# Performance work log

Measured on AMD Instinct MI355X. Metric: run time of the kernel, lower is better.

## Reference

```python
import jax, jax.numpy as jnp
import numpy as np

B, T, D = 128, 512, 400
N_VALS, N_ACTS = 1024, 128

def setup_inputs() -> dict:
    key = jax.random.key(0)
    ks = jax.random.split(key, 7)
    H_utt = jax.random.normal(ks[0], (B, T, D), dtype=jnp.float32)
    c_utt = jax.random.normal(ks[1], (B, D), dtype=jnp.float32)
    C_acts = jax.random.normal(ks[2], (B, N_ACTS, D), dtype=jnp.float32)
    C_vals = jax.random.normal(ks[3], (N_VALS, 1, D), dtype=jnp.float32)
    W_score = jax.random.normal(ks[4], (1, D), dtype=jnp.float32) * (1.0 / np.sqrt(D))
    b_score = jnp.zeros((1,), dtype=jnp.float32)
    lens = jax.random.randint(ks[5], (B,), T // 2, T + 1, dtype=jnp.int64 if jax.config.read('jax_enable_x64') else jnp.int32)
    lens = lens.at[0].set(T)  # ensure max(lens) == T so masking matches torch semantics
    return {"H_utt": H_utt, "c_utt": c_utt, "C_acts": C_acts, "C_vals": C_vals,
            "W_score": W_score, "b_score": b_score, "utterance_len": lens}

def reference(H_utt, c_utt, C_acts, C_vals, W_score, b_score, utterance_len):
    vals = C_vals[:, 0, :]                                   # [V, D]
    # --- y_utts: default attention of each value vector over utterance states ---
    scores = jnp.einsum('btd,vd->bvt', H_utt, vals)          # mul+sum scoring
    mask = jnp.arange(T)[None, :] < utterance_len[:, None]   # [B, T]
    scores = jnp.where(mask[:, None, :], scores, -jnp.inf)
    probs = jax.nn.softmax(scores, axis=-1)                  # [B, V, T]
    q_utts = jnp.einsum('bvt,btd->bvd', probs, H_utt)        # weighted sum contexts
    y_utts = jnp.einsum('bvd,d->bv', q_utts, W_score[0]) + b_score[0]  # utt_scorer
    # --- y_acts: attention of c_utt over per-example act vectors, then score vs vals ---
    s2 = jnp.einsum('bad,bd->ba', C_acts, c_utt)
    p2 = jax.nn.softmax(s2, axis=-1)
    q_acts = jnp.einsum('ba,bad->bd', p2, C_acts)            # [B, D]
    y_acts = q_acts @ vals.T                                 # [B, V]
    return (y_utts, y_acts)
```

## Files before the change

### kernel.cpp

```cpp
#include <hip/hip_runtime.h>
#include <hip/hip_bf16.h>

#define B_  128
#define T_  512
#define D_  400
#define NV  1024
#define NA  128

#define TILE_BYTES 13312
#define MAIN_BLOCKS 512

#define LDH  424
#define NT   32
#define FB_MAIN_BLOCKS 1024

typedef __bf16 bf16_t;
typedef bf16_t bf16x8 __attribute__((ext_vector_type(8)));
typedef bf16_t bf16x4 __attribute__((ext_vector_type(4)));
typedef float  floatx4 __attribute__((ext_vector_type(4)));

__device__ inline float dot4(float4 a, float4 b) {
    return a.x * b.x + a.y * b.y + a.z * b.z + a.w * b.w;
}

__global__ __launch_bounds__(256) void prep_kernel(const float* __restrict__ H,
                                                   const float* __restrict__ W,
                                                   const float* __restrict__ Ca,
                                                   const float* __restrict__ cu,
                                                   float* __restrict__ hw,
                                                   bf16_t* __restrict__ Hf,
                                                   float* __restrict__ s2) {
    int wave = threadIdx.x >> 6;
    int lane = threadIdx.x & 63;
    if (blockIdx.x < 1024) {
        int tile = blockIdx.x * 4 + wave;
        int b = tile >> 5, ti = tile & 31;
        int lrow = lane & 15, quad = lane >> 4;
        const float* hrow = H + ((size_t)b * T_ + ti * 16 + lrow) * D_;
        char* fdst = (char*)Hf + (size_t)tile * TILE_BYTES + lane * 16;
        float acc = 0.f;
#pragma unroll
        for (int kk = 0; kk < 13; ++kk) {
            int k0 = kk * 32 + quad * 8;
            bf16x8 f;
            if (k0 < D_) {
                float4 x = *(const float4*)(hrow + k0);
                float4 y = *(const float4*)(hrow + k0 + 4);
                float4 wx = *(const float4*)(W + k0);
                float4 wy = *(const float4*)(W + k0 + 4);
                acc += dot4(x, wx) + dot4(y, wy);
                f[0] = (bf16_t)x.x; f[1] = (bf16_t)x.y; f[2] = (bf16_t)x.z; f[3] = (bf16_t)x.w;
                f[4] = (bf16_t)y.x; f[5] = (bf16_t)y.y; f[6] = (bf16_t)y.z; f[7] = (bf16_t)y.w;
            } else {
#pragma unroll
                for (int j = 0; j < 8; ++j) f[j] = (bf16_t)0.0f;
            }
            *(bf16x8*)(fdst + kk * 1024) = f;
        }
        acc += __shfl_xor(acc, 16, 64);
        acc += __shfl_xor(acc, 32, 64);
        if (lane < 16) hw[b * T_ + ti * 16 + lane] = acc;
    } else {
        long row = (long)(blockIdx.x - 1024) * 4 + wave;
        int b = (int)(row >> 7);
        const float4* a4 = (const float4*)(Ca + row * (long)D_);
        const float4* c4 = (const float4*)(cu + (long)b * D_);
        float acc = dot4(a4[lane], c4[lane]);
        if (lane < 36) acc += dot4(a4[lane + 64], c4[lane + 64]);
#pragma unroll
        for (int off = 1; off < 64; off <<= 1) acc += __shfl_xor(acc, off, 64);
        if (lane == 0) s2[row] = acc;
    }
}

__global__ __launch_bounds__(256) void qacts_kernel(const float* __restrict__ s2,
                                                    const float* __restrict__ Ca,
                                                    float* __restrict__ q_ws) {
    __shared__ float p_lds[NA];
    __shared__ float red[8];
    __shared__ __align__(16) float4 part[100];
    int b = blockIdx.x;
    int tid = threadIdx.x, wave = tid >> 6, lane = tid & 63;

    float s = (tid < NA) ? s2[(long)b * NA + tid] : -3.0e38f;
    float m = s;
#pragma unroll
    for (int off = 1; off < 64; off <<= 1) m = fmaxf(m, __shfl_xor(m, off, 64));
    if (lane == 0) red[wave] = m;
    __syncthreads();
    m = fmaxf(red[0], red[1]);
    float e = (tid < NA) ? __expf(s - m) : 0.f;
    float sum = e;
#pragma unroll
    for (int off = 1; off < 64; off <<= 1) sum += __shfl_xor(sum, off, 64);
    if (lane == 0) red[4 + wave] = sum;
    __syncthreads();
    float S = red[4] + red[5];
    if (tid < NA) p_lds[tid] = e / S;
    __syncthreads();

    int c4 = tid % 100;
    int half = tid / 100;
    float4 acc0 = {0.f, 0.f, 0.f, 0.f};
    if (tid < 200) {
        const float4* Cb4 = (const float4*)(Ca + (size_t)b * NA * D_);
        float4 acc1 = {0.f, 0.f, 0.f, 0.f};
        int a0 = half * 64;
#pragma unroll 4
        for (int a = 0; a < 64; a += 2) {
            float p0 = p_lds[a0 + a], p1 = p_lds[a0 + a + 1];
            float4 x0 = Cb4[(size_t)(a0 + a) * 100 + c4];
            float4 x1 = Cb4[(size_t)(a0 + a + 1) * 100 + c4];
            acc0.x += p0 * x0.x; acc0.y += p0 * x0.y; acc0.z += p0 * x0.z; acc0.w += p0 * x0.w;
            acc1.x += p1 * x1.x; acc1.y += p1 * x1.y; acc1.z += p1 * x1.z; acc1.w += p1 * x1.w;
        }
        acc0.x += acc1.x; acc0.y += acc1.y; acc0.z += acc1.z; acc0.w += acc1.w;
        if (half == 1) part[c4] = acc0;
    }
    __syncthreads();
    if (tid < 100) {
        float4 o = part[c4];
        o.x += acc0.x; o.y += acc0.y; o.z += acc0.z; o.w += acc0.w;
        ((float4*)(q_ws + (size_t)b * D_))[c4] = o;
    }
}

#define LDTILE(BUF, TI)                                                        \
    _Pragma("unroll") for (int kk = 0; kk < 13; ++kk)                          \
        BUF[kk] = *(const bf16x8*)(fb + (size_t)(TI) * TILE_BYTES + kk * 1024);

#define COMPUTE(BUF, TI)                                                       \
    do {                                                                       \
        floatx4 c_[4];                                                         \
        _Pragma("unroll") for (int s_ = 0; s_ < 4; ++s_) c_[s_] = zero4;       \
        _Pragma("unroll") for (int kk = 0; kk < 13; ++kk) {                    \
            bf16x8 bb_ = BUF[kk];                                              \
            _Pragma("unroll") for (int s_ = 0; s_ < 4; ++s_)                   \
                c_[s_] = __builtin_amdgcn_mfma_f32_16x16x32_bf16(              \
                    afrag[s_][kk], bb_, c_[s_], 0, 0, 0);                      \
        }                                                                      \
        int t_ = (TI) * 16 + lrow;                                             \
        float hwv_ = hwb[t_];                                                  \
        bool ok_ = t_ < len;                                                   \
        float cm_ = -3.0e38f;                                                  \
        _Pragma("unroll") for (int s_ = 0; s_ < 4; ++s_)                       \
            _Pragma("unroll") for (int r_ = 0; r_ < 4; ++r_) {                 \
                float v_ = ok_ ? c_[s_][r_] : -3.0e38f;                        \
                c_[s_][r_] = v_;                                               \
                cm_ = fmaxf(cm_, v_);                                          \
            }                                                                  \
        float mn_ = fmaxf(m_s, cm_);                                           \
        float alpha_ = __expf(m_s - mn_);                                      \
        m_s = mn_;                                                             \
        _Pragma("unroll") for (int s_ = 0; s_ < 4; ++s_)                       \
            _Pragma("unroll") for (int r_ = 0; r_ < 4; ++r_) {                 \
                float p_ = __expf(c_[s_][r_] - mn_);                           \
                l_s[s_][r_] = l_s[s_][r_] * alpha_ + p_;                       \
                a_s[s_][r_] = a_s[s_][r_] * alpha_ + p_ * hwv_;                \
            }                                                                  \
    } while (0)

__global__ __launch_bounds__(256, 1) void main_kernel(const bf16_t* __restrict__ Hf,
                                                      const float* __restrict__ Cv,
                                                      const float* __restrict__ hw,
                                                      const float* __restrict__ bs,
                                                      const int* __restrict__ lens,
                                                      const float* __restrict__ q_ws,
                                                      float* __restrict__ out) {
    int tid = threadIdx.x;
    int wave = tid >> 6, lane = tid & 63;

    if (blockIdx.x >= MAIN_BLOCKS) {
        long grp = (long)(blockIdx.x - MAIN_BLOCKS) * 4 + wave;
        int b = (int)(grp >> 8);
        int v0 = (int)(grp & 255) * 4;
        const float4* q4 = (const float4*)(q_ws + (size_t)b * D_);
        float4 qa = q4[lane];
        float4 qb = (lane < 36) ? q4[lane + 64] : make_float4(0.f, 0.f, 0.f, 0.f);
        float acc[4];
#pragma unroll
        for (int r = 0; r < 4; ++r) {
            const float4* v4 = (const float4*)(Cv + (size_t)(v0 + r) * D_);
            acc[r] = dot4(v4[lane], qa);
            if (lane < 36) acc[r] += dot4(v4[lane + 64], qb);
        }
#pragma unroll
        for (int off = 1; off < 64; off <<= 1) {
#pragma unroll
            for (int r = 0; r < 4; ++r) acc[r] += __shfl_xor(acc[r], off, 64);
        }
        if (lane == 0) {
            float4 o = make_float4(acc[0], acc[1], acc[2], acc[3]);
            *(float4*)(out + (size_t)B_ * NV + (size_t)b * NV + v0) = o;
        }
        return;
    }

    int i = blockIdx.x;
    int xcd = i & 7, vc = (i >> 3) & 3, bb = i >> 5;
    int b = xcd + 8 * bb;
    int vbase = vc * 256 + wave * 64;

    int lrow = lane & 15, quad = lane >> 4;
    int len = lens[b];
    float b0 = bs[0];

    bf16x8 afrag[4][13];
#pragma unroll
    for (int set = 0; set < 4; ++set) {
        const float* vrow = Cv + (size_t)(vbase + set * 16 + lrow) * D_;
#pragma unroll
        for (int kk = 0; kk < 13; ++kk) {
            int k0 = kk * 32 + quad * 8;
            bf16x8 f;
            if (k0 >= D_) {
#pragma unroll
                for (int j = 0; j < 8; ++j) f[j] = (bf16_t)0.0f;
            } else {
                const float4* p = (const float4*)(vrow + k0);
                float4 x = p[0], y = p[1];
                f[0] = (bf16_t)x.x; f[1] = (bf16_t)x.y;
                f[2] = (bf16_t)x.z; f[3] = (bf16_t)x.w;
                f[4] = (bf16_t)y.x; f[5] = (bf16_t)y.y;
                f[6] = (bf16_t)y.z; f[7] = (bf16_t)y.w;
            }
            afrag[set][kk] = f;
        }
    }

    float m_s = -3.0e38f;
    float l_s[4][4], a_s[4][4];
#pragma unroll
    for (int s = 0; s < 4; ++s)
#pragma unroll
        for (int r = 0; r < 4; ++r) { l_s[s][r] = 0.f; a_s[s][r] = 0.f; }

    const floatx4 zero4 = {0.f, 0.f, 0.f, 0.f};
    const float* hwb = hw + (size_t)b * T_;
    const char* fb = (const char*)Hf + (size_t)b * 32 * TILE_BYTES + lane * 16;

    int ntiles = (len + 15) >> 4;
    bf16x8 bfA[13], bfB[13];

    LDTILE(bfA, 0);
    int ti = 0;
    while (true) {
        if (ti + 1 < ntiles) { LDTILE(bfB, ti + 1); }
        COMPUTE(bfA, ti);
        ++ti; if (ti == ntiles) break;
        if (ti + 1 < ntiles) { LDTILE(bfA, ti + 1); }
        COMPUTE(bfB, ti);
        ++ti; if (ti == ntiles) break;
    }

#pragma unroll
    for (int s = 0; s < 4; ++s)
#pragma unroll
        for (int r = 0; r < 4; ++r) {
            float m = m_s, l = l_s[s][r], a = a_s[s][r];
#pragma unroll
            for (int off = 1; off < 16; off <<= 1) {
                float mo = __shfl_xor(m, off, 64);
                float lo = __shfl_xor(l, off, 64);
                float ao = __shfl_xor(a, off, 64);
                float mx = fmaxf(m, mo);
                float f1 = __expf(m - mx), f2 = __expf(mo - mx);
                l = l * f1 + lo * f2;
                a = a * f1 + ao * f2;
                m = mx;
            }
            if (lrow == 0) {
                int v = vbase + s * 16 + quad * 4 + r;
                out[(size_t)b * NV + v] = a / l + b0;
            }
        }
}

__global__ __launch_bounds__(256) void prep_fb_kernel(const float* __restrict__ H,
                                                      const float* __restrict__ W,
                                                      const float* __restrict__ Ca,
                                                      const float* __restrict__ cu,
                                                      float* __restrict__ hw,
                                                      float* __restrict__ s2) {
    int wave = threadIdx.x >> 6;
    int lane = threadIdx.x & 63;
    if (blockIdx.x < B_ * T_ / 4) {
        long row = (long)blockIdx.x * 4 + wave;
        const float* h = H + row * D_;
        float acc = 0.f;
        for (int k = lane; k < D_; k += 64) acc += h[k] * W[k];
#pragma unroll
        for (int off = 1; off < 64; off <<= 1) acc += __shfl_xor(acc, off, 64);
        if (lane == 0) hw[row] = acc;
    } else {
        long row = (long)(blockIdx.x - B_ * T_ / 4) * 4 + wave;
        int b = (int)(row >> 7);
        const float4* a4 = (const float4*)(Ca + row * (long)D_);
        const float4* c4 = (const float4*)(cu + (long)b * D_);
        float acc = dot4(a4[lane], c4[lane]);
        if (lane < 36) acc += dot4(a4[lane + 64], c4[lane + 64]);
#pragma unroll
        for (int off = 1; off < 64; off <<= 1) acc += __shfl_xor(acc, off, 64);
        if (lane == 0) s2[row] = acc;
    }
}

__global__ __launch_bounds__(256, 2) void main_fb_kernel(const float* __restrict__ H,
                                                         const float* __restrict__ Cv,
                                                         const float* __restrict__ hw,
                                                         const float* __restrict__ bs,
                                                         const int* __restrict__ lens,
                                                         const float* __restrict__ q_ws,
                                                         float* __restrict__ out) {
    __shared__ bf16_t h_lds[NT * LDH];
    __shared__ float hw_lds[NT];

    int tid = threadIdx.x;
    int wave = tid >> 6, lane = tid & 63;

    if (blockIdx.x >= FB_MAIN_BLOCKS) {
        long grp = (long)(blockIdx.x - FB_MAIN_BLOCKS) * 4 + wave;
        int b = (int)(grp >> 8);
        int v0 = (int)(grp & 255) * 4;
        const float4* q4 = (const float4*)(q_ws + (size_t)b * D_);
        float4 qa = q4[lane];
        float4 qb = (lane < 36) ? q4[lane + 64] : make_float4(0.f, 0.f, 0.f, 0.f);
        float acc[4];
#pragma unroll
        for (int r = 0; r < 4; ++r) {
            const float4* v4 = (const float4*)(Cv + (size_t)(v0 + r) * D_);
            acc[r] = dot4(v4[lane], qa);
            if (lane < 36) acc[r] += dot4(v4[lane + 64], qb);
        }
#pragma unroll
        for (int off = 1; off < 64; off <<= 1) {
#pragma unroll
            for (int r = 0; r < 4; ++r) acc[r] += __shfl_xor(acc[r], off, 64);
        }
        if (lane == 0) {
            float4 o = make_float4(acc[0], acc[1], acc[2], acc[3]);
            *(float4*)(out + (size_t)B_ * NV + (size_t)b * NV + v0) = o;
        }
        return;
    }

    int i = blockIdx.x;
    int xcd = i & 7, vc = (i >> 3) & 7, bb = i >> 6;
    int b = xcd + 8 * bb;
    int vbase = vc * 128;

    int lrow = lane & 15, quad = lane >> 4;
    int len = lens[b];
    float b0 = bs[0];

    for (int idx = tid; idx < NT * (LDH - D_); idx += 256) {
        int r = idx / (LDH - D_), c = idx % (LDH - D_);
        h_lds[r * LDH + D_ + c] = (bf16_t)0.0f;
    }

    bf16x8 afrag[2][13];
#pragma unroll
    for (int set = 0; set < 2; ++set) {
        const float* vrow = Cv + (size_t)(vbase + wave * 32 + set * 16 + lrow) * D_;
#pragma unroll
        for (int kk = 0; kk < 13; ++kk) {
            int k0 = kk * 32 + quad * 8;
            bf16x8 f;
            if (k0 >= D_) {
#pragma unroll
                for (int j = 0; j < 8; ++j) f[j] = (bf16_t)0.0f;
            } else {
                const float4* p = (const float4*)(vrow + k0);
                float4 x = p[0], y = p[1];
                f[0] = (bf16_t)x.x; f[1] = (bf16_t)x.y;
                f[2] = (bf16_t)x.z; f[3] = (bf16_t)x.w;
                f[4] = (bf16_t)y.x; f[5] = (bf16_t)y.y;
                f[6] = (bf16_t)y.z; f[7] = (bf16_t)y.w;
            }
            afrag[set][kk] = f;
        }
    }

    float m_s = -3.0e38f;
    float l_s[2][4], a_s[2][4];
#pragma unroll
    for (int set = 0; set < 2; ++set)
#pragma unroll
        for (int r = 0; r < 4; ++r) { l_s[set][r] = 0.f; a_s[set][r] = 0.f; }

    int ntiles = (len + NT - 1) / NT;
    const float* Hb = H + (size_t)b * T_ * D_;

    for (int tt = 0; tt < ntiles; ++tt) {
        int t0 = tt * NT;
        __syncthreads();
        for (int idx = tid; idx < NT * (D_ / 4); idx += 256) {
            int r = idx / (D_ / 4), c4 = idx % (D_ / 4);
            float4 x = *(const float4*)(Hb + (size_t)(t0 + r) * D_ + c4 * 4);
            bf16x4 f;
            f[0] = (bf16_t)x.x; f[1] = (bf16_t)x.y;
            f[2] = (bf16_t)x.z; f[3] = (bf16_t)x.w;
            *(bf16x4*)(&h_lds[r * LDH + c4 * 4]) = f;
        }
        if (tid < NT) hw_lds[tid] = hw[(size_t)b * T_ + t0 + tid];
        __syncthreads();

        floatx4 c[2][2];
        floatx4 zero4 = {0.f, 0.f, 0.f, 0.f};
#pragma unroll
        for (int set = 0; set < 2; ++set)
#pragma unroll
            for (int s = 0; s < 2; ++s) c[set][s] = zero4;

#pragma unroll
        for (int kk = 0; kk < 13; ++kk) {
            int koff = kk * 32 + quad * 8;
#pragma unroll
            for (int s = 0; s < 2; ++s) {
                bf16x8 bfr = *(const bf16x8*)(&h_lds[(s * 16 + lrow) * LDH + koff]);
                c[0][s] = __builtin_amdgcn_mfma_f32_16x16x32_bf16(afrag[0][kk], bfr, c[0][s], 0, 0, 0);
                c[1][s] = __builtin_amdgcn_mfma_f32_16x16x32_bf16(afrag[1][kk], bfr, c[1][s], 0, 0, 0);
            }
        }

        if (t0 + NT > len) {
#pragma unroll
            for (int s = 0; s < 2; ++s) {
                int t = t0 + s * 16 + lrow;
                if (t >= len) {
#pragma unroll
                    for (int set = 0; set < 2; ++set) {
                        c[set][s][0] = -3.0e38f; c[set][s][1] = -3.0e38f;
                        c[set][s][2] = -3.0e38f; c[set][s][3] = -3.0e38f;
                    }
                }
            }
        }

        float hw0 = hw_lds[lrow], hw1 = hw_lds[16 + lrow];
        float cm = -3.0e38f;
#pragma unroll
        for (int set = 0; set < 2; ++set)
#pragma unroll
            for (int s = 0; s < 2; ++s)
#pragma unroll
                for (int r = 0; r < 4; ++r) cm = fmaxf(cm, c[set][s][r]);
        float mn = fmaxf(m_s, cm);
        float alpha = __expf(m_s - mn);
        m_s = mn;
#pragma unroll
        for (int set = 0; set < 2; ++set)
#pragma unroll
            for (int r = 0; r < 4; ++r) {
                float p0 = __expf(c[set][0][r] - mn);
                float p1 = __expf(c[set][1][r] - mn);
                l_s[set][r] = l_s[set][r] * alpha + (p0 + p1);
                a_s[set][r] = a_s[set][r] * alpha + (p0 * hw0 + p1 * hw1);
            }
    }

#pragma unroll
    for (int set = 0; set < 2; ++set)
#pragma unroll
        for (int r = 0; r < 4; ++r) {
            float m = m_s, l = l_s[set][r], a = a_s[set][r];
#pragma unroll
            for (int off = 1; off < 16; off <<= 1) {
                float mo = __shfl_xor(m, off, 64);
                float lo = __shfl_xor(l, off, 64);
                float ao = __shfl_xor(a, off, 64);
                float mx = fmaxf(m, mo);
                float f1 = __expf(m - mx), f2 = __expf(mo - mx);
                l = l * f1 + lo * f2;
                a = a * f1 + ao * f2;
                m = mx;
            }
            if (lrow == 0) {
                int v = vbase + wave * 32 + set * 16 + quad * 4 + r;
                out[(size_t)b * NV + v] = a / l + b0;
            }
        }
}

extern "C" void kernel_launch(void* const* d_in, const int* in_sizes, int n_in,
                              void* d_out, int out_size, void* d_ws, size_t ws_size,
                              hipStream_t stream) {
    const float* H    = (const float*)d_in[0];
    const float* cu   = (const float*)d_in[1];
    const float* Ca   = (const float*)d_in[2];
    const float* Cv   = (const float*)d_in[3];
    const float* W    = (const float*)d_in[4];
    const float* bs   = (const float*)d_in[5];
    const int*   lens = (const int*)d_in[6];
    float* out = (float*)d_out;

    float*  hw   = (float*)d_ws;
    float*  q_ws = hw + (size_t)B_ * T_;
    float*  s2   = q_ws + (size_t)B_ * D_;
    bf16_t* Hf   = (bf16_t*)(s2 + (size_t)B_ * NA);

    size_t need = ((size_t)B_ * T_ + (size_t)B_ * D_ + (size_t)B_ * NA) * sizeof(float)
                + (size_t)4096 * TILE_BYTES;
    bool pre = (ws_size >= need);

    if (pre) {
        prep_kernel<<<dim3(1024 + B_ * NA / 4), dim3(256), 0, stream>>>(H, W, Ca, cu, hw, Hf, s2);
        qacts_kernel<<<dim3(B_), dim3(256), 0, stream>>>(s2, Ca, q_ws);
        main_kernel<<<dim3(MAIN_BLOCKS + B_ * NV / 16), dim3(256), 0, stream>>>(Hf, Cv, hw, bs, lens, q_ws, out);
    } else {
        prep_fb_kernel<<<dim3(B_ * T_ / 4 + B_ * NA / 4), dim3(256), 0, stream>>>(H, W, Ca, cu, hw, s2);
        qacts_kernel<<<dim3(B_), dim3(256), 0, stream>>>(s2, Ca, q_ws);
        main_fb_kernel<<<dim3(FB_MAIN_BLOCKS + B_ * NV / 16), dim3(256), 0, stream>>>(H, Cv, hw, bs, lens, q_ws, out);
    }
}
```

Baseline: 314.4 us.

## Stage H tiles through LDS with async global_load_lds double buffering; split y_acts kernel

After: 298.8 us. 5.0% less time.

```diff
diff --git a/kernel.cpp b/kernel.cpp
--- a/kernel.cpp
+++ b/kernel.cpp
@@ -8,16 +8,23 @@
 #define NA  128
 
 #define TILE_BYTES 13312
-#define MAIN_BLOCKS 512
+#define STEP_BYTES 26624
+#define ATTN_BLOCKS 512
 
 #define LDH  424
-#define NT   32
+#define NT_FB 32
 #define FB_MAIN_BLOCKS 1024
 
 typedef __bf16 bf16_t;
 typedef bf16_t bf16x8 __attribute__((ext_vector_type(8)));
 typedef bf16_t bf16x4 __attribute__((ext_vector_type(4)));
 typedef float  floatx4 __attribute__((ext_vector_type(4)));
+
+__device__ inline void async_copy16(const void* g, void* l) {
+    __builtin_amdgcn_global_load_lds(
+        (const __attribute__((address_space(1))) unsigned int*)g,
+        (__attribute__((address_space(3))) unsigned int*)l, 16, 0, 0);
+}
 
 __device__ inline float dot4(float4 a, float4 b) {
     return a.x * b.x + a.y * b.y + a.z * b.z + a.w * b.w;
@@ -125,83 +132,52 @@
     }
 }
 
-#define LDTILE(BUF, TI)                                                        \
-    _Pragma("unroll") for (int kk = 0; kk < 13; ++kk)                          \
-        BUF[kk] = *(const bf16x8*)(fb + (size_t)(TI) * TILE_BYTES + kk * 1024);
-
-#define COMPUTE(BUF, TI)                                                       \
-    do {                                                                       \
-        floatx4 c_[4];                                                         \
-        _Pragma("unroll") for (int s_ = 0; s_ < 4; ++s_) c_[s_] = zero4;       \
-        _Pragma("unroll") for (int kk = 0; kk < 13; ++kk) {                    \
-            bf16x8 bb_ = BUF[kk];                                              \
-            _Pragma("unroll") for (int s_ = 0; s_ < 4; ++s_)                   \
-                c_[s_] = __builtin_amdgcn_mfma_f32_16x16x32_bf16(              \
-                    afrag[s_][kk], bb_, c_[s_], 0, 0, 0);                      \
-        }                                                                      \
-        int t_ = (TI) * 16 + lrow;                                             \
-        float hwv_ = hwb[t_];                                                  \
-        bool ok_ = t_ < len;                                                   \
-        float cm_ = -3.0e38f;                                                  \
-        _Pragma("unroll") for (int s_ = 0; s_ < 4; ++s_)                       \
-            _Pragma("unroll") for (int r_ = 0; r_ < 4; ++r_) {                 \
-                float v_ = ok_ ? c_[s_][r_] : -3.0e38f;                        \
-                c_[s_][r_] = v_;                                               \
-                cm_ = fmaxf(cm_, v_);                                          \
-            }                                                                  \
-        float mn_ = fmaxf(m_s, cm_);                                           \
-        float alpha_ = __expf(m_s - mn_);                                      \
-        m_s = mn_;                                                             \
-        _Pragma("unroll") for (int s_ = 0; s_ < 4; ++s_)                       \
-            _Pragma("unroll") for (int r_ = 0; r_ < 4; ++r_) {                 \
-                float p_ = __expf(c_[s_][r_] - mn_);                           \
-                l_s[s_][r_] = l_s[s_][r_] * alpha_ + p_;                       \
-                a_s[s_][r_] = a_s[s_][r_] * alpha_ + p_ * hwv_;                \
-            }                                                                  \
-    } while (0)
-
-__global__ __launch_bounds__(256, 1) void main_kernel(const bf16_t* __restrict__ Hf,
+__global__ __launch_bounds__(256) void yacts_kernel(const float* __restrict__ q_ws,
+                                                    const float* __restrict__ Cv,
+                                                    float* __restrict__ out) {
+    int wave = threadIdx.x >> 6;
+    int lane = threadIdx.x & 63;
+    long grp = (long)blockIdx.x * 4 + wave;
+    int b = (int)(grp >> 8);
+    int v0 = (int)(grp & 255) * 4;
+    const float4* q4 = (const float4*)(q_ws + (size_t)b * D_);
+    float4 qa = q4[lane];
+    float4 qb = (lane < 36) ? q4[lane + 64] : make_float4(0.f, 0.f, 0.f, 0.f);
+    float acc[4];
+#pragma unroll
+    for (int r = 0; r < 4; ++r) {
+        const float4* v4 = (const float4*)(Cv + (size_t)(v0 + r) * D_);
+        acc[r] = dot4(v4[lane], qa);
+        if (lane < 36) acc[r] += dot4(v4[lane + 64], qb);
+    }
+#pragma unroll
+    for (int off = 1; off < 64; off <<= 1) {
+#pragma unroll
+        for (int r = 0; r < 4; ++r) acc[r] += __shfl_xor(acc[r], off, 64);
+    }
+    if (lane == 0) {
+        float4 o = make_float4(acc[0], acc[1], acc[2], acc[3]);
+        *(float4*)(out + (size_t)B_ * NV + (size_t)b * NV + v0) = o;
+    }
+}
+
+__global__ __launch_bounds__(256, 1) void attn_kernel(const bf16_t* __restrict__ Hf,
                                                       const float* __restrict__ Cv,
                                                       const float* __restrict__ hw,
                                                       const float* __restrict__ bs,
                                                       const int* __restrict__ lens,
-                                                      const float* __restrict__ q_ws,
                                                       float* __restrict__ out) {
+    __shared__ __align__(16) char lds[2][STEP_BYTES];
+
     int tid = threadIdx.x;
     int wave = tid >> 6, lane = tid & 63;
-
-    if (blockIdx.x >= MAIN_BLOCKS) {
-        long grp = (long)(blockIdx.x - MAIN_BLOCKS) * 4 + wave;
-        int b = (int)(grp >> 8);
-        int v0 = (int)(grp & 255) * 4;
-        const float4* q4 = (const float4*)(q_ws + (size_t)b * D_);
-        float4 qa = q4[lane];
-        float4 qb = (lane < 36) ? q4[lane + 64] : make_float4(0.f, 0.f, 0.f, 0.f);
-        float acc[4];
-#pragma unroll
-        for (int r = 0; r < 4; ++r) {
-            const float4* v4 = (const float4*)(Cv + (size_t)(v0 + r) * D_);
-            acc[r] = dot4(v4[lane], qa);
-            if (lane < 36) acc[r] += dot4(v4[lane + 64], qb);
-        }
-#pragma unroll
-        for (int off = 1; off < 64; off <<= 1) {
-#pragma unroll
-            for (int r = 0; r < 4; ++r) acc[r] += __shfl_xor(acc[r], off, 64);
-        }
-        if (lane == 0) {
-            float4 o = make_float4(acc[0], acc[1], acc[2], acc[3]);
-            *(float4*)(out + (size_t)B_ * NV + (size_t)b * NV + v0) = o;
-        }
-        return;
-    }
+    int lrow = lane & 15, quad = lane >> 4;
 
     int i = blockIdx.x;
     int xcd = i & 7, vc = (i >> 3) & 3, bb = i >> 5;
     int b = xcd + 8 * bb;
     int vbase = vc * 256 + wave * 64;
 
-    int lrow = lane & 15, quad = lane >> 4;
     int len = lens[b];
     float b0 = bs[0];
 
@@ -235,29 +211,85 @@
 #pragma unroll
         for (int r = 0; r < 4; ++r) { l_s[s][r] = 0.f; a_s[s][r] = 0.f; }
 
-    const floatx4 zero4 = {0.f, 0.f, 0.f, 0.f};
+    const char* fb = (const char*)Hf + (size_t)b * 32 * TILE_BYTES;
     const float* hwb = hw + (size_t)b * T_;
-    const char* fb = (const char*)Hf + (size_t)b * 32 * TILE_BYTES + lane * 16;
-
-    int ntiles = (len + 15) >> 4;
-    bf16x8 bfA[13], bfB[13];
-
-    LDTILE(bfA, 0);
-    int ti = 0;
-    while (true) {
-        if (ti + 1 < ntiles) { LDTILE(bfB, ti + 1); }
-        COMPUTE(bfA, ti);
-        ++ti; if (ti == ntiles) break;
-        if (ti + 1 < ntiles) { LDTILE(bfA, ti + 1); }
-        COMPUTE(bfB, ti);
-        ++ti; if (ti == ntiles) break;
-    }
-
-#pragma unroll
-    for (int s = 0; s < 4; ++s)
+    int nsteps = (len + 31) >> 5;
+
+#pragma unroll 1
+    for (int c = wave; c < 26; c += 4)
+        async_copy16(fb + c * 1024 + lane * 16, lds[0] + c * 1024 + lane * 16);
+
+    for (int tt = 0; tt < nsteps; ++tt) {
+        __syncthreads();
+        if (tt + 1 < nsteps) {
+            const char* gs = fb + (size_t)(tt + 1) * STEP_BYTES;
+            char* ls = lds[(tt + 1) & 1];
+#pragma unroll 1
+            for (int c = wave; c < 26; c += 4)
+                async_copy16(gs + c * 1024 + lane * 16, ls + c * 1024 + lane * 16);
+        }
+
+        const char* lb = lds[tt & 1] + lane * 16;
+        floatx4 c[4][2];
+        const floatx4 zero4 = {0.f, 0.f, 0.f, 0.f};
+#pragma unroll
+        for (int s = 0; s < 4; ++s) { c[s][0] = zero4; c[s][1] = zero4; }
+
+#pragma unroll
+        for (int kk = 0; kk < 13; ++kk) {
+            bf16x8 b0 = *(const bf16x8*)(lb + kk * 1024);
+            bf16x8 b1 = *(const bf16x8*)(lb + TILE_BYTES + kk * 1024);
+#pragma unroll
+            for (int set = 0; set < 4; ++set) {
+                c[set][0] = __builtin_amdgcn_mfma_f32_16x16x32_bf16(afrag[set][kk], b0, c[set][0], 0, 0, 0);
+                c[set][1] = __builtin_amdgcn_mfma_f32_16x16x32_bf16(afrag[set][kk], b1, c[set][1], 0, 0, 0);
+            }
+        }
+
+        int t0 = tt * 32;
+        if (t0 + 32 > len) {
+#pragma unroll
+            for (int s = 0; s < 2; ++s) {
+                int t = t0 + s * 16 + lrow;
+                if (t >= len) {
+#pragma unroll
+                    for (int set = 0; set < 4; ++set) {
+                        c[set][s][0] = -3.0e38f; c[set][s][1] = -3.0e38f;
+                        c[set][s][2] = -3.0e38f; c[set][s][3] = -3.0e38f;
+                    }
+                }
+            }
+        }
+
+        float hw0 = hwb[t0 + lrow];
+        float hw1 = hwb[t0 + 16 + lrow];
+
+        float cm = -3.0e38f;
+#pragma unroll
+        for (int set = 0; set < 4; ++set)
+#pragma unroll
+            for (int s = 0; s < 2; ++s)
+#pragma unroll
+                for (int r = 0; r < 4; ++r) cm = fmaxf(cm, c[set][s][r]);
+        float mn = fmaxf(m_s, cm);
+        float alpha = __expf(m_s - mn);
+        m_s = mn;
+#pragma unroll
+        for (int set = 0; set < 4; ++set)
+#pragma unroll
+            for (int r = 0; r < 4; ++r) {
+                float p0 = __expf(c[set][0][r] - mn);
+                float p1 = __expf(c[set][1][r] - mn);
+                l_s[set][r] = l_s[set][r] * alpha + (p0 + p1);
+                a_s[set][r] = a_s[set][r] * alpha + (p0 * hw0 + p1 * hw1);
+            }
+    }
+
+#pragma unroll
+    for (int set = 0; set < 4; ++set)
 #pragma unroll
         for (int r = 0; r < 4; ++r) {
-            float m = m_s, l = l_s[s][r], a = a_s[s][r];
+            float m = m_s, l = l_s[set][r], a = a_s[set][r];
 #pragma unroll
             for (int off = 1; off < 16; off <<= 1) {
                 float mo = __shfl_xor(m, off, 64);
@@ -270,7 +302,7 @@
                 m = mx;
             }
             if (lrow == 0) {
-                int v = vbase + s * 16 + quad * 4 + r;
+                int v = vbase + set * 16 + quad * 4 + r;
                 out[(size_t)b * NV + v] = a / l + b0;
             }
         }
@@ -310,39 +342,12 @@
                                                          const float* __restrict__ hw,
                                                          const float* __restrict__ bs,
                                                          const int* __restrict__ lens,
-                                                         const float* __restrict__ q_ws,
                                                          float* __restrict__ out) {
-    __shared__ bf16_t h_lds[NT * LDH];
-    __shared__ float hw_lds[NT];
+    __shared__ bf16_t h_lds[NT_FB * LDH];
+    __shared__ float hw_lds[NT_FB];
 
     int tid = threadIdx.x;
     int wave = tid >> 6, lane = tid & 63;
-
-    if (blockIdx.x >= FB_MAIN_BLOCKS) {
-        long grp = (long)(blockIdx.x - FB_MAIN_BLOCKS) * 4 + wave;
-        int b = (int)(grp >> 8);
-        int v0 = (int)(grp & 255) * 4;
-        const float4* q4 = (const float4*)(q_ws + (size_t)b * D_);
-        float4 qa = q4[lane];
-        float4 qb = (lane < 36) ? q4[lane + 64] : make_float4(0.f, 0.f, 0.f, 0.f);
-        float acc[4];
-#pragma unroll
-        for (int r = 0; r < 4; ++r) {
-            const float4* v4 = (const float4*)(Cv + (size_t)(v0 + r) * D_);
-            acc[r] = dot4(v4[lane], qa);
-            if (lane < 36) acc[r] += dot4(v4[lane + 64], qb);
-        }
-#pragma unroll
-        for (int off = 1; off < 64; off <<= 1) {
-#pragma unroll
-            for (int r = 0; r < 4; ++r) acc[r] += __shfl_xor(acc[r], off, 64);
-        }
-        if (lane == 0) {
-            float4 o = make_float4(acc[0], acc[1], acc[2], acc[3]);
-            *(float4*)(out + (size_t)B_ * NV + (size_t)b * NV + v0) = o;
-        }
-        return;
-    }
 
     int i = blockIdx.x;
     int xcd = i & 7, vc = (i >> 3) & 7, bb = i >> 6;
@@ -353,7 +358,7 @@
     int len = lens[b];
     float b0 = bs[0];
 
-    for (int idx = tid; idx < NT * (LDH - D_); idx += 256) {
+    for (int idx = tid; idx < NT_FB * (LDH - D_); idx += 256) {
         int r = idx / (LDH - D_), c = idx % (LDH - D_);
         h_lds[r * LDH + D_ + c] = (bf16_t)0.0f;
     }
@@ -388,13 +393,13 @@
 #pragma unroll
         for (int r = 0; r < 4; ++r) { l_s[set][r] = 0.f; a_s[set][r] = 0.f; }
 
-    int ntiles = (len + NT - 1) / NT;
+    int ntiles = (len + NT_FB - 1) / NT_FB;
     const float* Hb = H + (size_t)b * T_ * D_;
 
     for (int tt = 0; tt < ntiles; ++tt) {
-        int t0 = tt * NT;
+        int t0 = tt * NT_FB;
         __syncthreads();
-        for (int idx = tid; idx < NT * (D_ / 4); idx += 256) {
+        for (int idx = tid; idx < NT_FB * (D_ / 4); idx += 256) {
             int r = idx / (D_ / 4), c4 = idx % (D_ / 4);
             float4 x = *(const float4*)(Hb + (size_t)(t0 + r) * D_ + c4 * 4);
             bf16x4 f;
@@ -402,7 +407,7 @@
             f[2] = (bf16_t)x.z; f[3] = (bf16_t)x.w;
             *(bf16x4*)(&h_lds[r * LDH + c4 * 4]) = f;
         }
-        if (tid < NT) hw_lds[tid] = hw[(size_t)b * T_ + t0 + tid];
+        if (tid < NT_FB) hw_lds[tid] = hw[(size_t)b * T_ + t0 + tid];
         __syncthreads();
 
         floatx4 c[2][2];
@@ -423,7 +428,7 @@
             }
         }
 
-        if (t0 + NT > len) {
+        if (t0 + NT_FB > len) {
 #pragma unroll
             for (int s = 0; s < 2; ++s) {
                 int t = t0 + s * 16 + lrow;
@@ -506,10 +511,12 @@
     if (pre) {
         prep_kernel<<<dim3(1024 + B_ * NA / 4), dim3(256), 0, stream>>>(H, W, Ca, cu, hw, Hf, s2);
         qacts_kernel<<<dim3(B_), dim3(256), 0, stream>>>(s2, Ca, q_ws);
-        main_kernel<<<dim3(MAIN_BLOCKS + B_ * NV / 16), dim3(256), 0, stream>>>(Hf, Cv, hw, bs, lens, q_ws, out);
+        attn_kernel<<<dim3(ATTN_BLOCKS), dim3(256), 0, stream>>>(Hf, Cv, hw, bs, lens, out);
+        yacts_kernel<<<dim3(B_ * NV / 16), dim3(256), 0, stream>>>(q_ws, Cv, out);
     } else {
         prep_fb_kernel<<<dim3(B_ * T_ / 4 + B_ * NA / 4), dim3(256), 0, stream>>>(H, W, Ca, cu, hw, s2);
         qacts_kernel<<<dim3(B_), dim3(256), 0, stream>>>(s2, Ca, q_ws);
-        main_fb_kernel<<<dim3(FB_MAIN_BLOCKS + B_ * NV / 16), dim3(256), 0, stream>>>(H, Cv, hw, bs, lens, q_ws, out);
-    }
-}
+        main_fb_kernel<<<dim3(FB_MAIN_BLOCKS), dim3(256), 0, stream>>>(H, Cv, hw, bs, lens, out);
+        yacts_kernel<<<dim3(B_ * NV / 16), dim3(256), 0, stream>>>(q_ws, Cv, out);
+    }
+}
```
